# Kernel optimization log

Measured on AMD Instinct MI355X. Metric: run time of the kernel, lower is better.

The kernel has to match this reference:

```python
import jax, jax.numpy as jnp
import numpy as np

N = 100000
E = 1600000
D_IN, D_HID, D_OUT = 128, 128, 64
EPS = 1e-5


def setup_inputs() -> dict:
    key = jax.random.key(0)
    ks = jax.random.split(key, 16)
    inp = {
        "x": jax.random.normal(ks[0], (N, D_IN), dtype=jnp.float32),
        "edge_index": jax.random.randint(ks[1], (2, E), 0, N, dtype=jnp.int64),
        # layer 1: SAGEConv(D_IN -> D_HID)
        "w_l1": jax.random.normal(ks[2], (D_HID, D_IN), dtype=jnp.float32) / np.sqrt(D_IN),
        "b_l1": jnp.zeros((D_HID,), dtype=jnp.float32),
        "w_r1": jax.random.normal(ks[3], (D_HID, D_IN), dtype=jnp.float32) / np.sqrt(D_IN),
        "bn1_gamma": jnp.ones((D_HID,), dtype=jnp.float32),
        "bn1_beta": jnp.zeros((D_HID,), dtype=jnp.float32),
        "bn1_mean": jnp.zeros((D_HID,), dtype=jnp.float32),
        "bn1_var": jnp.ones((D_HID,), dtype=jnp.float32),
        # layer 2: SAGEConv(D_HID -> D_HID)
        "w_l2": jax.random.normal(ks[4], (D_HID, D_HID), dtype=jnp.float32) / np.sqrt(D_HID),
        "b_l2": jnp.zeros((D_HID,), dtype=jnp.float32),
        "w_r2": jax.random.normal(ks[5], (D_HID, D_HID), dtype=jnp.float32) / np.sqrt(D_HID),
        "bn2_gamma": jnp.ones((D_HID,), dtype=jnp.float32),
        "bn2_beta": jnp.zeros((D_HID,), dtype=jnp.float32),
        "bn2_mean": jnp.zeros((D_HID,), dtype=jnp.float32),
        "bn2_var": jnp.ones((D_HID,), dtype=jnp.float32),
        # layer 3: SAGEConv(D_HID -> D_OUT)
        "w_l3": jax.random.normal(ks[6], (D_OUT, D_HID), dtype=jnp.float32) / np.sqrt(D_HID),
        "b_l3": jnp.zeros((D_OUT,), dtype=jnp.float32),
        "w_r3": jax.random.normal(ks[7], (D_OUT, D_HID), dtype=jnp.float32) / np.sqrt(D_HID),
    }
    return inp


def _sage_conv(x, src, dst, w_l, b_l, w_r):
    """PyG SAGEConv default: mean-aggregate source features into targets,
    then lin_l(aggr) + lin_r(root). w_* are [out,in] (torch layout)."""
    msgs = x[src]                                   # [E, d]  gather
    agg = jax.ops.segment_sum(msgs, dst, num_segments=N)   # [N, d] scatter-add
    deg = jax.ops.segment_sum(jnp.ones((src.shape[0],), x.dtype), dst, num_segments=N)
    agg = agg / jnp.maximum(deg, 1.0)[:, None]      # mean (0 for isolated nodes)
    return agg @ w_l.T + b_l + x @ w_r.T


def _bn_eval(x, gamma, beta, mean, var):
    return (x - mean) * (gamma * jax.lax.rsqrt(var + EPS)) + beta


def reference(x, edge_index,
              w_l1, b_l1, w_r1, bn1_gamma, bn1_beta, bn1_mean, bn1_var,
              w_l2, b_l2, w_r2, bn2_gamma, bn2_beta, bn2_mean, bn2_var,
              w_l3, b_l3, w_r3):
    src, dst = edge_index[0], edge_index[1]
    h = _sage_conv(x, src, dst, w_l1, b_l1, w_r1)
    h = jax.nn.relu(_bn_eval(h, bn1_gamma, bn1_beta, bn1_mean, bn1_var))
    h = _sage_conv(h, src, dst, w_l2, b_l2, w_r2)
    h = jax.nn.relu(_bn_eval(h, bn2_gamma, bn2_beta, bn2_mean, bn2_var))
    h = _sage_conv(h, src, dst, w_l3, b_l3, w_r3)
    return h
```

## Files before the change

### kernel.cpp

```cpp
#include <hip/hip_runtime.h>

#define N_NODES 100000
#define N_EDGES 1600000
#define D 128
#define EPS 1e-5f

#define NPB_BITS 8
#define NODES_PER_BUCK 256
#define NBUCK ((N_NODES + NODES_PER_BUCK - 1) >> NPB_BITS)
#define BUCK_CAP 5120

#define CHUNK_E 8192
#define NB_BIN ((N_EDGES + CHUNK_E - 1) / CHUNK_E)

typedef unsigned int uint;
typedef unsigned short ushort;
using bf16x8 = __attribute__((ext_vector_type(8))) short;
using f32x4  = __attribute__((ext_vector_type(4))) float;

__device__ __forceinline__ ushort f2bf(float f) {
    uint u = __float_as_uint(f);
    return (ushort)((u + 0x7fffu + ((u >> 16) & 1u)) >> 16);
}
__device__ __forceinline__ float bflo(uint u) { return __uint_as_float(u << 16); }
__device__ __forceinline__ float bfhi(uint u) { return __uint_as_float(u & 0xffff0000u); }


__global__ __launch_bounds__(256) void k_bhist(const int* __restrict__ ei, int* __restrict__ bcnt) {
    __shared__ int sc[NBUCK];
    int t = threadIdx.x;
    for (int i = t; i < NBUCK; i += 256) sc[i] = 0;
    __syncthreads();
    int stride = gridDim.x * 256;
    for (int e = blockIdx.x * 256 + t; e < N_EDGES; e += stride)
        atomicAdd(&sc[ei[N_EDGES + e] >> NPB_BITS], 1);
    __syncthreads();
    for (int i = t; i < NBUCK; i += 256) {
        int v = sc[i];
        if (v) atomicAdd(&bcnt[i], v);
    }
}

__global__ __launch_bounds__(1024) void k_bscan(const int* __restrict__ bcnt,
                                                int* __restrict__ bstart, int* __restrict__ bcur,
                                                int* __restrict__ row_start) {
    __shared__ int s[1024];
    int t = threadIdx.x;
    int own = (t < NBUCK) ? bcnt[t] : 0;
    s[t] = own;
    __syncthreads();
    for (int off = 1; off < 1024; off <<= 1) {
        int v = (t >= off) ? s[t - off] : 0;
        __syncthreads();
        s[t] += v;
        __syncthreads();
    }
    if (t < NBUCK) {
        int excl = s[t] - own;
        bstart[t] = excl;
        bcur[t] = excl;
    }
    if (t == 0) {
        bstart[NBUCK] = N_EDGES;
        row_start[N_NODES] = N_EDGES;
    }
}

__global__ __launch_bounds__(256) void k_bin2(const int* __restrict__ ei,
                                              int* __restrict__ bcur,
                                              uint* __restrict__ binned) {
    __shared__ int cnt[NBUCK];
    __shared__ int base[NBUCK];
    int t = threadIdx.x;
    int e0 = blockIdx.x * CHUNK_E;
    int e1 = e0 + CHUNK_E; if (e1 > N_EDGES) e1 = N_EDGES;
    for (int i = t; i < NBUCK; i += 256) cnt[i] = 0;
    __syncthreads();
    for (int e = e0 + t; e < e1; e += 256)
        atomicAdd(&cnt[ei[N_EDGES + e] >> NPB_BITS], 1);
    __syncthreads();
    for (int i = t; i < NBUCK; i += 256) {
        int v = cnt[i];
        base[i] = v ? atomicAdd(&bcur[i], v) : 0;
        cnt[i] = 0;
    }
    __syncthreads();
    for (int e = e0 + t; e < e1; e += 256) {
        int s = ei[e];
        int d = ei[N_EDGES + e];
        int b = d >> NPB_BITS;
        int pos = base[b] + atomicAdd(&cnt[b], 1);
        binned[pos] = ((uint)s << NPB_BITS) | (uint)(d & (NODES_PER_BUCK - 1));
    }
}

__global__ __launch_bounds__(256) void k_bcsr(const uint* __restrict__ binned,
                                              const int* __restrict__ bstart,
                                              int* __restrict__ row_start,
                                              int* __restrict__ csr_src) {
    __shared__ int cnt[NODES_PER_BUCK];
    __shared__ int sc[NODES_PER_BUCK];
    __shared__ int cur[NODES_PER_BUCK];
    __shared__ uint ecache[BUCK_CAP];
    int b = blockIdx.x, t = threadIdx.x;
    int s0 = bstart[b], s1 = bstart[b + 1];
    cnt[t] = 0;
    __syncthreads();
    for (int e = s0 + t; e < s1; e += 256) {
        uint u = binned[e];
        int idx = e - s0;
        if (idx < BUCK_CAP) ecache[idx] = u;
        atomicAdd(&cnt[u & (NODES_PER_BUCK - 1)], 1);
    }
    __syncthreads();
    int own = cnt[t];
    sc[t] = own;
    __syncthreads();
    for (int off = 1; off < NODES_PER_BUCK; off <<= 1) {
        int v = (t >= off) ? sc[t - off] : 0;
        __syncthreads();
        sc[t] += v;
        __syncthreads();
    }
    {
        int excl = s0 + sc[t] - own;
        int node = (b << NPB_BITS) + t;
        if (node < N_NODES) row_start[node] = excl;
        cur[t] = excl;
    }
    __syncthreads();
    for (int e = s0 + t; e < s1; e += 256) {
        int idx = e - s0;
        uint u = (idx < BUCK_CAP) ? ecache[idx] : binned[e];
        int pos = atomicAdd(&cur[u & (NODES_PER_BUCK - 1)], 1);
        csr_src[pos] = (int)(u >> NPB_BITS);
    }
}


__global__ void k_cast_x(const float* __restrict__ in, ushort* __restrict__ out, int n4) {
    int i = blockIdx.x * blockDim.x + threadIdx.x;
    if (i < n4) {
        float4 v = ((const float4*)in)[i];
        ushort4 o;
        o.x = f2bf(v.x); o.y = f2bf(v.y); o.z = f2bf(v.z); o.w = f2bf(v.w);
        ((ushort4*)out)[i] = o;
    }
}

__global__ void k_cast_w12(const float* __restrict__ Wl, const float* __restrict__ Wr,
                           ushort* __restrict__ W2) {
    int i = blockIdx.x * blockDim.x + threadIdx.x;
    if (i < 128 * 256) {
        int o = i >> 8, k = i & 255;
        float v = (k < 128) ? Wl[o * 128 + k] : Wr[o * 128 + (k - 128)];
        W2[i] = f2bf(v);
    }
}

__global__ void k_cast_w3(const float* __restrict__ Wl, const float* __restrict__ Wr,
                          ushort* __restrict__ W2) {
    int i = blockIdx.x * blockDim.x + threadIdx.x;
    if (i < 128 * D) {
        int o = i >> 7, k = i & 127;
        float v = (o < 64) ? Wl[o * D + k] : Wr[(o - 64) * D + k];
        W2[i] = f2bf(v);
    }
}

__global__ void k_bnprep(const float* __restrict__ bias, const float* __restrict__ gamma,
                         const float* __restrict__ beta, const float* __restrict__ mean,
                         const float* __restrict__ var,
                         float* __restrict__ A, float* __restrict__ B) {
    int c = threadIdx.x;
    float a = gamma[c] * rsqrtf(var[c] + EPS);
    A[c] = a;
    B[c] = (bias[c] - mean[c]) * a + beta[c];
}

__global__ __launch_bounds__(256) void k_agg_mean(
    const ushort* __restrict__ Zin, const int* __restrict__ row_start,
    const int* __restrict__ csr_src, ushort* __restrict__ Agg) {
    int t = threadIdx.x;
    int w = t >> 6, l = t & 63;
    int n = blockIdx.x * 4 + w;
    int g = l >> 3, c = l & 7;
    int s0 = row_start[n], s1 = row_start[n + 1];
    float a[16];
#pragma unroll
    for (int j = 0; j < 16; ++j) a[j] = 0.f;
    for (int e = s0; e < s1; e += 8) {
        int ee = e + g;
        if (ee < s1) {
            int src = csr_src[ee];
            const ushort* zp = &Zin[(size_t)src * 128 + c * 16];
            uint4 v0 = *(const uint4*)zp;
            uint4 v1 = *(const uint4*)(zp + 8);
            a[0] += bflo(v0.x); a[1] += bfhi(v0.x);
            a[2] += bflo(v0.y); a[3] += bfhi(v0.y);
            a[4] += bflo(v0.z); a[5] += bfhi(v0.z);
            a[6] += bflo(v0.w); a[7] += bfhi(v0.w);
            a[8]  += bflo(v1.x); a[9]  += bfhi(v1.x);
            a[10] += bflo(v1.y); a[11] += bfhi(v1.y);
            a[12] += bflo(v1.z); a[13] += bfhi(v1.z);
            a[14] += bflo(v1.w); a[15] += bfhi(v1.w);
        }
    }
#pragma unroll
    for (int off = 8; off <= 32; off <<= 1)
#pragma unroll
        for (int j = 0; j < 16; ++j) a[j] += __shfl_xor(a[j], off);
    if (l < 8) {
        float inv = 1.f / fmaxf((float)(s1 - s0), 1.f);
        uint4 p0, p1;
        uint* q0 = (uint*)&p0;
        uint* q1 = (uint*)&p1;
#pragma unroll
        for (int j = 0; j < 4; ++j) {
            q0[j] = (uint)f2bf(a[2 * j] * inv)     | ((uint)f2bf(a[2 * j + 1] * inv) << 16);
            q1[j] = (uint)f2bf(a[8 + 2 * j] * inv) | ((uint)f2bf(a[9 + 2 * j] * inv) << 16);
        }
        ushort* op = &Agg[(size_t)n * 128 + l * 16];
        *(uint4*)op = p0;
        *(uint4*)(op + 8) = p1;
    }
}

__global__ __launch_bounds__(256) void k_gemm12(
    const ushort* __restrict__ Ag, const ushort* __restrict__ Xin,
    const ushort* __restrict__ W2,
    const float* __restrict__ bnA, const float* __restrict__ bnB,
    ushort* __restrict__ Hout) {
    __shared__ ushort sW[16384];

    int t = threadIdx.x;
    int n0 = blockIdx.x * 64;
    int w = t >> 6, l = t & 63;

    int arow = n0 + 16 * w + (l & 15);
    if (arow >= N_NODES) arow = N_NODES - 1;
    int ko = (l >> 4) * 8;
    bf16x8 afr[8];
#pragma unroll
    for (int kt = 0; kt < 4; ++kt)
        afr[kt] = *(const bf16x8*)&Ag[(size_t)arow * 128 + kt * 32 + ko];
#pragma unroll
    for (int kt = 0; kt < 4; ++kt)
        afr[4 + kt] = *(const bf16x8*)&Xin[(size_t)arow * 128 + kt * 32 + ko];

    f32x4 acc[8];
#pragma unroll
    for (int ot = 0; ot < 8; ++ot) acc[ot] = (f32x4){0.f, 0.f, 0.f, 0.f};

#pragma unroll
    for (int p = 0; p < 2; ++p) {
        for (int s = t; s < 2048; s += 256) {
            int f = s >> 6, ln = s & 63;
            int o = (f >> 2) * 16 + (ln & 15);
            int k = p * 128 + (f & 3) * 32 + ((ln >> 4) * 8);
            *(uint4*)&sW[s * 8] = *(const uint4*)&W2[o * 256 + k];
        }
        __syncthreads();
#pragma unroll
        for (int ktl = 0; ktl < 4; ++ktl) {
            int kt = p * 4 + ktl;
#pragma unroll
            for (int ot = 0; ot < 8; ++ot) {
                bf16x8 bfr = *(const bf16x8*)&sW[((ot * 4 + ktl) * 64 + l) * 8];
                acc[ot] = __builtin_amdgcn_mfma_f32_16x16x32_bf16(afr[kt], bfr, acc[ot], 0, 0, 0);
            }
        }
        __syncthreads();
    }

    float* sC = (float*)sW;
    int r0 = (l >> 4) * 4;
#pragma unroll
    for (int ot = 0; ot < 8; ++ot)
#pragma unroll
        for (int j = 0; j < 4; ++j)
            sC[(16 * w + r0 + j) * 128 + ot * 16 + (l & 15)] = acc[ot][j];
    __syncthreads();

    for (int u = t; u < 1024; u += 256) {
        int r = u >> 4, cc = (u & 15) * 8;
        int n = n0 + r;
        if (n >= N_NODES) continue;
        float4 A0 = *(const float4*)&bnA[cc];
        float4 A1 = *(const float4*)&bnA[cc + 4];
        float4 B0 = *(const float4*)&bnB[cc];
        float4 B1 = *(const float4*)&bnB[cc + 4];
        const float* pa0 = (const float*)&A0;
        const float* pa1 = (const float*)&A1;
        const float* pb0 = (const float*)&B0;
        const float* pb1 = (const float*)&B1;
        uint4 pk;
        uint* pw = (uint*)&pk;
#pragma unroll
        for (int j = 0; j < 4; ++j) {
            int i0 = 2 * j, i1 = 2 * j + 1;
            float va = (i0 < 4) ? pa0[i0] : pa1[i0 - 4];
            float vb = (i0 < 4) ? pb0[i0] : pb1[i0 - 4];
            float wa = (i1 < 4) ? pa0[i1] : pa1[i1 - 4];
            float wb = (i1 < 4) ? pb0[i1] : pb1[i1 - 4];
            float h0 = fmaxf(sC[r * 128 + cc + i0] * va + vb, 0.f);
            float h1 = fmaxf(sC[r * 128 + cc + i1] * wa + wb, 0.f);
            pw[j] = (uint)f2bf(h0) | ((uint)f2bf(h1) << 16);
        }
        *(uint4*)&Hout[(size_t)n * 128 + cc] = pk;
    }
}

__global__ __launch_bounds__(256) void k_gemm3(
    const ushort* __restrict__ Xb, const ushort* __restrict__ W2,
    const float* __restrict__ bias,
    ushort* __restrict__ Zb, ushort* __restrict__ Yb) {
    constexpr int DOUT = 64;
    constexpr int NT = 128;
    constexpr int OT = 8;

    __shared__ ushort sW[OT * 4 * 64 * 8];

    int t = threadIdx.x;
    int n0 = blockIdx.x * 64;
    int w = t >> 6, l = t & 63;
    int arow = n0 + 16 * w + (l & 15);
    if (arow >= N_NODES) arow = N_NODES - 1;
    const ushort* ap = &Xb[(size_t)arow * D + ((l >> 4) * 8)];
    bf16x8 afr[4];
#pragma unroll
    for (int kt = 0; kt < 4; ++kt) afr[kt] = *(const bf16x8*)(ap + kt * 32);

    for (int s = t; s < OT * 4 * 64; s += 256) {
        int f = s >> 6, ln = s & 63;
        int o = (f >> 2) * 16 + (ln & 15);
        int k = (f & 3) * 32 + ((ln >> 4) * 8);
        *(uint4*)&sW[s * 8] = *(const uint4*)&W2[o * D + k];
    }
    __syncthreads();

    f32x4 acc[OT];
#pragma unroll
    for (int ot = 0; ot < OT; ++ot) acc[ot] = (f32x4){0.f, 0.f, 0.f, 0.f};
#pragma unroll
    for (int kt = 0; kt < 4; ++kt)
#pragma unroll
        for (int ot = 0; ot < OT; ++ot) {
            bf16x8 bfr = *(const bf16x8*)&sW[((ot * 4 + kt) * 64 + l) * 8];
            acc[ot] = __builtin_amdgcn_mfma_f32_16x16x32_bf16(afr[kt], bfr, acc[ot], 0, 0, 0);
        }
    __syncthreads();

    float* sC = (float*)sW;
    int r0 = (l >> 4) * 4;
#pragma unroll
    for (int ot = 0; ot < OT; ++ot)
#pragma unroll
        for (int j = 0; j < 4; ++j)
            sC[(16 * w + r0 + j) * NT + ot * 16 + (l & 15)] = acc[ot][j];
    __syncthreads();

    constexpr int CH = NT / 8;
    for (int c = t; c < 64 * CH; c += 256) {
        int r = c / CH, cc = (c % CH) * 8;
        if (n0 + r >= N_NODES) continue;
        bool isY = cc >= DOUT;
        uint4 pk;
        uint* pw = (uint*)&pk;
#pragma unroll
        for (int j = 0; j < 4; ++j) {
            float f0 = sC[r * NT + cc + 2 * j];
            float f1 = sC[r * NT + cc + 2 * j + 1];
            if (isY) {
                f0 += bias[cc - DOUT + 2 * j];
                f1 += bias[cc - DOUT + 2 * j + 1];
            }
            pw[j] = (uint)f2bf(f0) | ((uint)f2bf(f1) << 16);
        }
        if (isY) *(uint4*)&Yb[(size_t)(n0 + r) * DOUT + cc - DOUT] = pk;
        else     *(uint4*)&Zb[(size_t)(n0 + r) * DOUT + cc] = pk;
    }
}

__global__ __launch_bounds__(256) void k_agg3(
    const ushort* __restrict__ Zb, const int* __restrict__ row_start,
    const int* __restrict__ csr_src, const ushort* __restrict__ Yb,
    float* __restrict__ out) {
    int t = threadIdx.x;
    int w = t >> 6, l = t & 63;
    int n = blockIdx.x * 4 + w;
    int g = l >> 3, c = l & 7;
    int s0 = row_start[n], s1 = row_start[n + 1];
    float a[8];
#pragma unroll
    for (int j = 0; j < 8; ++j) a[j] = 0.f;
    for (int e = s0; e < s1; e += 16) {
        int e0 = e + g, e1 = e + g + 8;
        int src0 = (e0 < s1) ? csr_src[e0] : -1;
        int src1 = (e1 < s1) ? csr_src[e1] : -1;
        uint4 v0, v1;
        if (src0 >= 0) v0 = *(const uint4*)&Zb[(size_t)src0 * 64 + c * 8];
        if (src1 >= 0) v1 = *(const uint4*)&Zb[(size_t)src1 * 64 + c * 8];
        if (src0 >= 0) {
            a[0] += bflo(v0.x); a[1] += bfhi(v0.x);
            a[2] += bflo(v0.y); a[3] += bfhi(v0.y);
            a[4] += bflo(v0.z); a[5] += bfhi(v0.z);
            a[6] += bflo(v0.w); a[7] += bfhi(v0.w);
        }
        if (src1 >= 0) {
            a[0] += bflo(v1.x); a[1] += bfhi(v1.x);
            a[2] += bflo(v1.y); a[3] += bfhi(v1.y);
            a[4] += bflo(v1.z); a[5] += bfhi(v1.z);
            a[6] += bflo(v1.w); a[7] += bfhi(v1.w);
        }
    }
#pragma unroll
    for (int off = 8; off <= 32; off <<= 1)
#pragma unroll
        for (int j = 0; j < 8; ++j) a[j] += __shfl_xor(a[j], off);
    if (l < 8) {
        float inv = 1.f / fmaxf((float)(s1 - s0), 1.f);
        uint4 yv = *(const uint4*)&Yb[(size_t)n * 64 + l * 8];
        float4 o0, o1;
        o0.x = bflo(yv.x) + a[0] * inv; o0.y = bfhi(yv.x) + a[1] * inv;
        o0.z = bflo(yv.y) + a[2] * inv; o0.w = bfhi(yv.y) + a[3] * inv;
        o1.x = bflo(yv.z) + a[4] * inv; o1.y = bfhi(yv.z) + a[5] * inv;
        o1.z = bflo(yv.w) + a[6] * inv; o1.w = bfhi(yv.w) + a[7] * inv;
        float* po = &out[(size_t)n * 64 + l * 8];
        *(float4*)po = o0;
        *(float4*)(po + 4) = o1;
    }
}


static inline size_t align256(size_t x) { return (x + 255) & ~(size_t)255; }

extern "C" void kernel_launch(void* const* d_in, const int* in_sizes, int n_in,
                              void* d_out, int out_size, void* d_ws, size_t ws_size,
                              hipStream_t stream) {
    const float* x    = (const float*)d_in[0];
    const int*   ei   = (const int*)d_in[1];
    const float* w_l1 = (const float*)d_in[2];
    const float* b_l1 = (const float*)d_in[3];
    const float* w_r1 = (const float*)d_in[4];
    const float* g1   = (const float*)d_in[5];
    const float* be1  = (const float*)d_in[6];
    const float* m1   = (const float*)d_in[7];
    const float* v1   = (const float*)d_in[8];
    const float* w_l2 = (const float*)d_in[9];
    const float* b_l2 = (const float*)d_in[10];
    const float* w_r2 = (const float*)d_in[11];
    const float* g2   = (const float*)d_in[12];
    const float* be2  = (const float*)d_in[13];
    const float* m2   = (const float*)d_in[14];
    const float* v2   = (const float*)d_in[15];
    const float* w_l3 = (const float*)d_in[16];
    const float* b_l3 = (const float*)d_in[17];
    const float* w_r3 = (const float*)d_in[18];
    float* out = (float*)d_out;

    char* w = (char*)d_ws;
    int* bcnt      = (int*)w;  w += align256((size_t)NBUCK * 4);
    int* bstart    = (int*)w;  w += align256((size_t)(NBUCK + 1) * 4);
    int* bcur      = (int*)w;  w += align256((size_t)NBUCK * 4);
    uint* binned   = (uint*)w; w += align256((size_t)N_EDGES * 4);
    int* row_start = (int*)w;  w += align256((size_t)(N_NODES + 1) * 4);
    int* csr_src   = (int*)w;  w += align256((size_t)N_EDGES * 4);
    ushort* xb     = (ushort*)w; w += align256((size_t)N_NODES * D * 2);
    ushort* ag     = (ushort*)w; w += align256((size_t)N_NODES * D * 2);
    ushort* h1     = (ushort*)w; w += align256((size_t)N_NODES * D * 2);
    ushort* h2     = (ushort*)w; w += align256((size_t)N_NODES * D * 2);
    ushort* Zb     = (ushort*)w; w += align256((size_t)N_NODES * 64 * 2);
    ushort* Yb     = (ushort*)w; w += align256((size_t)N_NODES * 64 * 2);
    ushort* w2_1   = (ushort*)w; w += align256((size_t)128 * 256 * 2);
    ushort* w2_2   = (ushort*)w; w += align256((size_t)128 * 256 * 2);
    ushort* w2_3   = (ushort*)w; w += align256((size_t)128 * 128 * 2);
    float* bnA1    = (float*)w;  w += align256(128 * 4);
    float* bnB1    = (float*)w;  w += align256(128 * 4);
    float* bnA2    = (float*)w;  w += align256(128 * 4);
    float* bnB2    = (float*)w;  w += align256(128 * 4);

    hipMemsetAsync(bcnt, 0, (size_t)NBUCK * 4, stream);

    k_bhist<<<256, 256, 0, stream>>>(ei, bcnt);
    k_bscan<<<1, 1024, 0, stream>>>(bcnt, bstart, bcur, row_start);
    k_bin2<<<NB_BIN, 256, 0, stream>>>(ei, bcur, binned);
    k_bcsr<<<NBUCK, 256, 0, stream>>>(binned, bstart, row_start, csr_src);

    int n4 = N_NODES * D / 4;
    k_cast_x<<<(n4 + 255) / 256, 256, 0, stream>>>(x, xb, n4);
    k_cast_w12<<<(128 * 256 + 255) / 256, 256, 0, stream>>>(w_l1, w_r1, w2_1);
    k_cast_w12<<<(128 * 256 + 255) / 256, 256, 0, stream>>>(w_l2, w_r2, w2_2);
    k_cast_w3<<<(128 * 128 + 255) / 256, 256, 0, stream>>>(w_l3, w_r3, w2_3);
    k_bnprep<<<1, 128, 0, stream>>>(b_l1, g1, be1, m1, v1, bnA1, bnB1);
    k_bnprep<<<1, 128, 0, stream>>>(b_l2, g2, be2, m2, v2, bnA2, bnB2);

    int gb = (N_NODES + 63) / 64;
    int ab = N_NODES / 4;

    k_agg_mean<<<ab, 256, 0, stream>>>(xb, row_start, csr_src, ag);
    k_gemm12<<<gb, 256, 0, stream>>>(ag, xb, w2_1, bnA1, bnB1, h1);
    k_agg_mean<<<ab, 256, 0, stream>>>(h1, row_start, csr_src, ag);
    k_gemm12<<<gb, 256, 0, stream>>>(ag, h1, w2_2, bnA2, bnB2, h2);
    k_gemm3<<<gb, 256, 0, stream>>>(h2, w2_3, b_l3, Zb, Yb);
    k_agg3<<<ab, 256, 0, stream>>>(Zb, row_start, csr_src, Yb, out);
}
```

Before: 327.3 us.

## Split mean-aggregation across two channel halves with two edges per lane in flight

The mean aggregation kernel now launches twice as many blocks, and each block handles one 64-channel half of the rows for four nodes. Each lane loads two edges' 16-byte slices per iteration instead of one edge's 32-byte slice. This halves per-thread accumulator registers and reduction shuffles and raises occupancy and memory-level parallelism for the gather. The cost is that each node's row_start and csr_src entries are read twice, and each gathered 256-byte row is split into 128-byte pieces fetched by different blocks.

```diff
diff --git a/kernel.cpp b/kernel.cpp
--- a/kernel.cpp
+++ b/kernel.cpp
@@ -183,46 +183,47 @@
     const int* __restrict__ csr_src, ushort* __restrict__ Agg) {
     int t = threadIdx.x;
     int w = t >> 6, l = t & 63;
-    int n = blockIdx.x * 4 + w;
+    int b = blockIdx.x;
+    int h = b & 1;
+    int n = (b >> 1) * 4 + w;
     int g = l >> 3, c = l & 7;
     int s0 = row_start[n], s1 = row_start[n + 1];
-    float a[16];
-#pragma unroll
-    for (int j = 0; j < 16; ++j) a[j] = 0.f;
-    for (int e = s0; e < s1; e += 8) {
-        int ee = e + g;
-        if (ee < s1) {
-            int src = csr_src[ee];
-            const ushort* zp = &Zin[(size_t)src * 128 + c * 16];
-            uint4 v0 = *(const uint4*)zp;
-            uint4 v1 = *(const uint4*)(zp + 8);
+    int choff = h * 64 + c * 8;
+    float a[8];
+#pragma unroll
+    for (int j = 0; j < 8; ++j) a[j] = 0.f;
+    for (int e = s0; e < s1; e += 16) {
+        int e0 = e + g, e1 = e + g + 8;
+        int src0 = (e0 < s1) ? csr_src[e0] : -1;
+        int src1 = (e1 < s1) ? csr_src[e1] : -1;
+        uint4 v0, v1;
+        if (src0 >= 0) v0 = *(const uint4*)&Zin[(size_t)src0 * 128 + choff];
+        if (src1 >= 0) v1 = *(const uint4*)&Zin[(size_t)src1 * 128 + choff];
+        if (src0 >= 0) {
             a[0] += bflo(v0.x); a[1] += bfhi(v0.x);
             a[2] += bflo(v0.y); a[3] += bfhi(v0.y);
             a[4] += bflo(v0.z); a[5] += bfhi(v0.z);
             a[6] += bflo(v0.w); a[7] += bfhi(v0.w);
-            a[8]  += bflo(v1.x); a[9]  += bfhi(v1.x);
-            a[10] += bflo(v1.y); a[11] += bfhi(v1.y);
-            a[12] += bflo(v1.z); a[13] += bfhi(v1.z);
-            a[14] += bflo(v1.w); a[15] += bfhi(v1.w);
+        }
+        if (src1 >= 0) {
+            a[0] += bflo(v1.x); a[1] += bfhi(v1.x);
+            a[2] += bflo(v1.y); a[3] += bfhi(v1.y);
+            a[4] += bflo(v1.z); a[5] += bfhi(v1.z);
+            a[6] += bflo(v1.w); a[7] += bfhi(v1.w);
         }
     }
 #pragma unroll
     for (int off = 8; off <= 32; off <<= 1)
 #pragma unroll
-        for (int j = 0; j < 16; ++j) a[j] += __shfl_xor(a[j], off);
+        for (int j = 0; j < 8; ++j) a[j] += __shfl_xor(a[j], off);
     if (l < 8) {
         float inv = 1.f / fmaxf((float)(s1 - s0), 1.f);
-        uint4 p0, p1;
-        uint* q0 = (uint*)&p0;
-        uint* q1 = (uint*)&p1;
-#pragma unroll
-        for (int j = 0; j < 4; ++j) {
-            q0[j] = (uint)f2bf(a[2 * j] * inv)     | ((uint)f2bf(a[2 * j + 1] * inv) << 16);
-            q1[j] = (uint)f2bf(a[8 + 2 * j] * inv) | ((uint)f2bf(a[9 + 2 * j] * inv) << 16);
-        }
-        ushort* op = &Agg[(size_t)n * 128 + l * 16];
-        *(uint4*)op = p0;
-        *(uint4*)(op + 8) = p1;
+        uint4 pk;
+        uint* q = (uint*)&pk;
+#pragma unroll
+        for (int j = 0; j < 4; ++j)
+            q[j] = (uint)f2bf(a[2 * j] * inv) | ((uint)f2bf(a[2 * j + 1] * inv) << 16);
+        *(uint4*)&Agg[(size_t)n * 128 + h * 64 + l * 8] = pk;
     }
 }
 
@@ -497,10 +498,11 @@
 
     int gb = (N_NODES + 63) / 64;
     int ab = N_NODES / 4;
-
-    k_agg_mean<<<ab, 256, 0, stream>>>(xb, row_start, csr_src, ag);
+    int ab2 = (N_NODES / 4) * 2;
+
+    k_agg_mean<<<ab2, 256, 0, stream>>>(xb, row_start, csr_src, ag);
     k_gemm12<<<gb, 256, 0, stream>>>(ag, xb, w2_1, bnA1, bnB1, h1);
-    k_agg_mean<<<ab, 256, 0, stream>>>(h1, row_start, csr_src, ag);
+    k_agg_mean<<<ab2, 256, 0, stream>>>(h1, row_start, csr_src, ag);
     k_gemm12<<<gb, 256, 0, stream>>>(ag, h1, w2_2, bnA2, bnB2, h2);
     k_gemm3<<<gb, 256, 0, stream>>>(h2, w2_3, b_l3, Zb, Yb);
     k_agg3<<<ab, 256, 0, stream>>>(Zb, row_start, csr_src, Yb, out);
```

New measurement: 347.9 us. 6.3% more time.

## Stage binned edges in LDS for coalesced writes and fuse cast/prep kernels

Applied to the files above, without the earlier changes.

k_bin2 now sorts each chunk's edges locally in shared memory by bucket and then writes them out contiguously, replacing scattered global writes with coalesced ones. k_bcsr likewise builds the per-bucket CSR in shared memory when the bucket fits and copies it out linearly. The six small cast and batchnorm-prep kernels are merged into one k_misc launch to cut launch overhead. The change raises shared-memory use per block (about 40KB in k_bin2), which may lower occupancy.

```diff
diff --git a/kernel.cpp b/kernel.cpp
--- a/kernel.cpp
+++ b/kernel.cpp
@@ -70,18 +70,37 @@
                                               int* __restrict__ bcur,
                                               uint* __restrict__ binned) {
     __shared__ int cnt[NBUCK];
-    __shared__ int base[NBUCK];
+    __shared__ int lbase[NBUCK];
+    __shared__ int gbase[NBUCK];
+    __shared__ int ssc[512];
+    __shared__ uint sval[CHUNK_E];
+    __shared__ ushort sbkt[CHUNK_E];
     int t = threadIdx.x;
     int e0 = blockIdx.x * CHUNK_E;
     int e1 = e0 + CHUNK_E; if (e1 > N_EDGES) e1 = N_EDGES;
+    int ecnt = e1 - e0;
     for (int i = t; i < NBUCK; i += 256) cnt[i] = 0;
     __syncthreads();
     for (int e = e0 + t; e < e1; e += 256)
         atomicAdd(&cnt[ei[N_EDGES + e] >> NPB_BITS], 1);
     __syncthreads();
+    int v0 = (t < NBUCK) ? cnt[t] : 0;
+    int v1 = (t + 256 < NBUCK) ? cnt[t + 256] : 0;
+    ssc[t] = v0; ssc[t + 256] = v1;
+    __syncthreads();
+    for (int off = 1; off < 512; off <<= 1) {
+        int a0 = (t >= off) ? ssc[t - off] : 0;
+        int a1 = (t + 256 >= off) ? ssc[t + 256 - off] : 0;
+        __syncthreads();
+        ssc[t] += a0; ssc[t + 256] += a1;
+        __syncthreads();
+    }
+    if (t < NBUCK) lbase[t] = ssc[t] - v0;
+    if (t + 256 < NBUCK) lbase[t + 256] = ssc[t + 256] - v1;
+    __syncthreads();
     for (int i = t; i < NBUCK; i += 256) {
         int v = cnt[i];
-        base[i] = v ? atomicAdd(&bcur[i], v) : 0;
+        gbase[i] = v ? atomicAdd(&bcur[i], v) : 0;
         cnt[i] = 0;
     }
     __syncthreads();
@@ -89,8 +108,14 @@
         int s = ei[e];
         int d = ei[N_EDGES + e];
         int b = d >> NPB_BITS;
-        int pos = base[b] + atomicAdd(&cnt[b], 1);
-        binned[pos] = ((uint)s << NPB_BITS) | (uint)(d & (NODES_PER_BUCK - 1));
+        int pos = lbase[b] + atomicAdd(&cnt[b], 1);
+        sval[pos] = ((uint)s << NPB_BITS) | (uint)(d & (NODES_PER_BUCK - 1));
+        sbkt[pos] = (ushort)b;
+    }
+    __syncthreads();
+    for (int s = t; s < ecnt; s += 256) {
+        int b = sbkt[s];
+        binned[gbase[b] + (s - lbase[b])] = sval[s];
     }
 }
 
@@ -102,8 +127,11 @@
     __shared__ int sc[NODES_PER_BUCK];
     __shared__ int cur[NODES_PER_BUCK];
     __shared__ uint ecache[BUCK_CAP];
+    __shared__ int sorted[BUCK_CAP];
     int b = blockIdx.x, t = threadIdx.x;
     int s0 = bstart[b], s1 = bstart[b + 1];
+    int m = s1 - s0;
+    bool fits = (m <= BUCK_CAP);
     cnt[t] = 0;
     __syncthreads();
     for (int e = s0 + t; e < s1; e += 256) {
@@ -122,60 +150,71 @@
         sc[t] += v;
         __syncthreads();
     }
+    int lexcl = sc[t] - own;
     {
-        int excl = s0 + sc[t] - own;
         int node = (b << NPB_BITS) + t;
-        if (node < N_NODES) row_start[node] = excl;
-        cur[t] = excl;
-    }
-    __syncthreads();
-    for (int e = s0 + t; e < s1; e += 256) {
-        int idx = e - s0;
-        uint u = (idx < BUCK_CAP) ? ecache[idx] : binned[e];
-        int pos = atomicAdd(&cur[u & (NODES_PER_BUCK - 1)], 1);
-        csr_src[pos] = (int)(u >> NPB_BITS);
-    }
-}
-
-
-__global__ void k_cast_x(const float* __restrict__ in, ushort* __restrict__ out, int n4) {
-    int i = blockIdx.x * blockDim.x + threadIdx.x;
-    if (i < n4) {
-        float4 v = ((const float4*)in)[i];
+        if (node < N_NODES) row_start[node] = s0 + lexcl;
+        cur[t] = fits ? lexcl : (s0 + lexcl);
+    }
+    __syncthreads();
+    if (fits) {
+        for (int e = s0 + t; e < s1; e += 256) {
+            uint u = ecache[e - s0];
+            int pos = atomicAdd(&cur[u & (NODES_PER_BUCK - 1)], 1);
+            sorted[pos] = (int)(u >> NPB_BITS);
+        }
+        __syncthreads();
+        for (int s = t; s < m; s += 256)
+            csr_src[s0 + s] = sorted[s];
+    } else {
+        for (int e = s0 + t; e < s1; e += 256) {
+            uint u = (e - s0 < BUCK_CAP) ? ecache[e - s0] : binned[e];
+            int pos = atomicAdd(&cur[u & (NODES_PER_BUCK - 1)], 1);
+            csr_src[pos] = (int)(u >> NPB_BITS);
+        }
+    }
+}
+
+__global__ __launch_bounds__(256) void k_misc(
+    const float* __restrict__ x, ushort* __restrict__ xb,
+    const float* __restrict__ wl1, const float* __restrict__ wr1, ushort* __restrict__ w21,
+    const float* __restrict__ wl2, const float* __restrict__ wr2, ushort* __restrict__ w22,
+    const float* __restrict__ wl3, const float* __restrict__ wr3, ushort* __restrict__ w23,
+    const float* __restrict__ b1, const float* __restrict__ g1, const float* __restrict__ be1,
+    const float* __restrict__ m1, const float* __restrict__ v1,
+    float* __restrict__ bnA1, float* __restrict__ bnB1,
+    const float* __restrict__ b2, const float* __restrict__ g2, const float* __restrict__ be2,
+    const float* __restrict__ m2, const float* __restrict__ v2,
+    float* __restrict__ bnA2, float* __restrict__ bnB2) {
+    int b = blockIdx.x, t = threadIdx.x;
+    if (b < 12500) {
+        int i = b * 256 + t;
+        float4 v = ((const float4*)x)[i];
         ushort4 o;
         o.x = f2bf(v.x); o.y = f2bf(v.y); o.z = f2bf(v.z); o.w = f2bf(v.w);
-        ((ushort4*)out)[i] = o;
-    }
-}
-
-__global__ void k_cast_w12(const float* __restrict__ Wl, const float* __restrict__ Wr,
-                           ushort* __restrict__ W2) {
-    int i = blockIdx.x * blockDim.x + threadIdx.x;
-    if (i < 128 * 256) {
+        ((ushort4*)xb)[i] = o;
+    } else if (b < 12628) {
+        int i = (b - 12500) * 256 + t;
         int o = i >> 8, k = i & 255;
-        float v = (k < 128) ? Wl[o * 128 + k] : Wr[o * 128 + (k - 128)];
-        W2[i] = f2bf(v);
-    }
-}
-
-__global__ void k_cast_w3(const float* __restrict__ Wl, const float* __restrict__ Wr,
-                          ushort* __restrict__ W2) {
-    int i = blockIdx.x * blockDim.x + threadIdx.x;
-    if (i < 128 * D) {
+        w21[i] = f2bf((k < 128) ? wl1[o * 128 + k] : wr1[o * 128 + k - 128]);
+    } else if (b < 12756) {
+        int i = (b - 12628) * 256 + t;
+        int o = i >> 8, k = i & 255;
+        w22[i] = f2bf((k < 128) ? wl2[o * 128 + k] : wr2[o * 128 + k - 128]);
+    } else if (b < 12820) {
+        int i = (b - 12756) * 256 + t;
         int o = i >> 7, k = i & 127;
-        float v = (o < 64) ? Wl[o * D + k] : Wr[(o - 64) * D + k];
-        W2[i] = f2bf(v);
-    }
-}
-
-__global__ void k_bnprep(const float* __restrict__ bias, const float* __restrict__ gamma,
-                         const float* __restrict__ beta, const float* __restrict__ mean,
-                         const float* __restrict__ var,
-                         float* __restrict__ A, float* __restrict__ B) {
-    int c = threadIdx.x;
-    float a = gamma[c] * rsqrtf(var[c] + EPS);
-    A[c] = a;
-    B[c] = (bias[c] - mean[c]) * a + beta[c];
+        w23[i] = f2bf((o < 64) ? wl3[o * 128 + k] : wr3[(o - 64) * 128 + k]);
+    } else {
+        if (t < 128) {
+            float a = g1[t] * rsqrtf(v1[t] + EPS);
+            bnA1[t] = a; bnB1[t] = (b1[t] - m1[t]) * a + be1[t];
+        } else {
+            int c = t - 128;
+            float a = g2[c] * rsqrtf(v2[c] + EPS);
+            bnA2[c] = a; bnB2[c] = (b2[c] - m2[c]) * a + be2[c];
+        }
+    }
 }
 
 __global__ __launch_bounds__(256) void k_agg_mean(
@@ -487,13 +526,10 @@
     k_bin2<<<NB_BIN, 256, 0, stream>>>(ei, bcur, binned);
     k_bcsr<<<NBUCK, 256, 0, stream>>>(binned, bstart, row_start, csr_src);
 
-    int n4 = N_NODES * D / 4;
-    k_cast_x<<<(n4 + 255) / 256, 256, 0, stream>>>(x, xb, n4);
-    k_cast_w12<<<(128 * 256 + 255) / 256, 256, 0, stream>>>(w_l1, w_r1, w2_1);
-    k_cast_w12<<<(128 * 256 + 255) / 256, 256, 0, stream>>>(w_l2, w_r2, w2_2);
-    k_cast_w3<<<(128 * 128 + 255) / 256, 256, 0, stream>>>(w_l3, w_r3, w2_3);
-    k_bnprep<<<1, 128, 0, stream>>>(b_l1, g1, be1, m1, v1, bnA1, bnB1);
-    k_bnprep<<<1, 128, 0, stream>>>(b_l2, g2, be2, m2, v2, bnA2, bnB2);
+    k_misc<<<12821, 256, 0, stream>>>(x, xb,
+        w_l1, w_r1, w2_1, w_l2, w_r2, w2_2, w_l3, w_r3, w2_3,
+        b_l1, g1, be1, m1, v1, bnA1, bnB1,
+        b_l2, g2, be2, m2, v2, bnA2, bnB2);
 
     int gb = (N_NODES + 63) / 64;
     int ab = N_NODES / 4;
```

Result: faster. 311.4 us (-4.9%).
